# Performance work log

Hardware: AMD Instinct MI355X
Metric: run time of the kernel (lower is better)

## Reference

```python
import jax, jax.numpy as jnp
import numpy as np

D = 2048        # hidden_size
F = 1024        # moe_intermediate_size
E = 16          # num_experts
TOP_K = 2       # num_experts_per_tok
NORM_TOPK = True
B, S = 2, 1024


def setup_inputs() -> dict:
    key = jax.random.key(0)
    ks = jax.random.split(key, 6)
    scale = 0.02
    x = jax.random.normal(ks[0], (B, S, D), jnp.float32)
    w_gate = jax.random.normal(ks[1], (D, E), jnp.float32) * scale          # gate Linear (no bias)
    w_g = jax.random.normal(ks[2], (E, D, F), jnp.float32) * scale          # SwitchGLU gate_proj
    w_u = jax.random.normal(ks[3], (E, D, F), jnp.float32) * scale          # SwitchGLU up_proj
    w_d = jax.random.normal(ks[4], (E, F, D), jnp.float32) * scale          # SwitchGLU down_proj
    expert_bias = jnp.zeros((E,), jnp.float32)                              # nn.Parameter(zeros)
    return {"x": x, "w_gate": w_gate, "w_g": w_g, "w_u": w_u, "w_d": w_d,
            "expert_bias": expert_bias}


def reference(x, w_gate, w_g, w_u, w_d, expert_bias):
    xf = x.reshape(-1, D)  # [T, D] flatten tokens
    T = xf.shape[0]
    # routing: softmax in fp32, bias added AFTER softmax (as in source)
    gates = jax.nn.softmax((xf @ w_gate).astype(jnp.float32), axis=-1) + expert_bias
    scores, inds = jax.lax.top_k(gates, TOP_K)  # values gathered from biased gates
    if NORM_TOPK:
        scores = scores / (jnp.sum(scores, axis=-1, keepdims=True) + 1e-20)
    scores = scores.astype(x.dtype)
    # scatter top-k weights into dense [T, E] combine matrix (top-k inds are distinct)
    cw = jnp.zeros((T, E), x.dtype).at[jnp.arange(T)[:, None], inds].add(scores)
    # scan over experts: each step one gated-SiLU MLP + weighted accumulate
    def step(acc, inp):
        wg, wu, wd, w = inp  # wg/wu [D,F], wd [F,D], w [T]
        h = jax.nn.silu(xf @ wg) * (xf @ wu)  # [T, F]
        return acc + w[:, None] * (h @ wd), None
    y, _ = jax.lax.scan(step, jnp.zeros_like(xf), (w_g, w_u, w_d, cw.T))
    return y.reshape(x.shape)
```

## Files before the change

kernel.cpp:

```cpp
#include <hip/hip_runtime.h>
#include <hip/hip_bf16.h>

#define D_DIM 2048
#define F_DIM 1024
#define E_NUM 16
#define T_TOK 2048
#define NSLOT (T_TOK * 2)

typedef float f32x4 __attribute__((ext_vector_type(4)));
typedef short short8 __attribute__((ext_vector_type(8)));

__device__ inline unsigned pk2bf(float a, float b) {
    __hip_bfloat162 h2 = __float22bfloat162_rn(make_float2(a, b));
    union { __hip_bfloat162 h; unsigned u; } c; c.h = h2; return c.u;
}

__global__ __launch_bounds__(64) void k_route(const float* __restrict__ x,
                                              const float* __restrict__ wg,
                                              const float* __restrict__ bias,
                                              int* __restrict__ topk_idx,
                                              float* __restrict__ topk_w,
                                              int* __restrict__ counts) {
    int t = blockIdx.x;
    int l = threadIdx.x;
    int e = l & 15, c = l >> 4;
    const float* xr = x + (size_t)t * D_DIM + c * (D_DIM / 4);
    const float* wr = wg + (size_t)(c * (D_DIM / 4)) * E_NUM + e;
    float acc = 0.f;
#pragma unroll 4
    for (int d = 0; d < D_DIM / 4; ++d) acc += xr[d] * wr[(size_t)d * E_NUM];
    acc += __shfl_xor(acc, 16);
    acc += __shfl_xor(acc, 32);
    float m = acc;
#pragma unroll
    for (int s = 1; s < 16; s <<= 1) m = fmaxf(m, __shfl_xor(m, s));
    float p = __expf(acc - m);
    float sum = p;
#pragma unroll
    for (int s = 1; s < 16; s <<= 1) sum += __shfl_xor(sum, s);
    p = p / sum + bias[e];
    float v1 = p; int i1 = e;
#pragma unroll
    for (int s = 1; s < 16; s <<= 1) {
        float ov = __shfl_xor(v1, s); int oi = __shfl_xor(i1, s);
        if (ov > v1 || (ov == v1 && oi < i1)) { v1 = ov; i1 = oi; }
    }
    float v2 = (e == i1) ? -1e30f : p; int i2 = e;
#pragma unroll
    for (int s = 1; s < 16; s <<= 1) {
        float ov = __shfl_xor(v2, s); int oi = __shfl_xor(i2, s);
        if (ov > v2 || (ov == v2 && oi < i2)) { v2 = ov; i2 = oi; }
    }
    if (l == 0) {
        float s2 = v1 + v2 + 1e-20f;
        topk_idx[2 * t] = i1; topk_idx[2 * t + 1] = i2;
        topk_w[2 * t] = v1 / s2; topk_w[2 * t + 1] = v2 / s2;
        atomicAdd(&counts[i1], 1);
        atomicAdd(&counts[i2], 1);
    }
}

__global__ void k_offsets(const int* __restrict__ counts, int* __restrict__ offsets,
                          int* __restrict__ cursors) {
    if (threadIdx.x == 0) {
        int run = 0;
        for (int e = 0; e < E_NUM; ++e) { offsets[e] = run; cursors[e] = run; run += counts[e]; }
        offsets[E_NUM] = run;
    }
}

__global__ void k_scatter(const int* __restrict__ topk_idx, const float* __restrict__ topk_w,
                          int* __restrict__ cursors, int* __restrict__ token_ids,
                          float* __restrict__ slot_w) {
    int i = blockIdx.x * blockDim.x + threadIdx.x;
    if (i >= NSLOT) return;
    int e = topk_idx[i];
    int slot = atomicAdd(&cursors[e], 1);
    token_ids[slot] = i >> 1;
    slot_w[slot] = topk_w[i];
}

__global__ __launch_bounds__(256) void k_gather(const float* __restrict__ x,
                                                const int* __restrict__ token_ids,
                                                __hip_bfloat16* __restrict__ xg) {
    int s = blockIdx.x;
    const float* src = x + (size_t)token_ids[s] * D_DIM + threadIdx.x * 8;
    f32x4 a = *(const f32x4*)src;
    f32x4 b = *(const f32x4*)(src + 4);
    union { short8 v; unsigned u[4]; } w;
    w.u[0] = pk2bf(a.x, a.y); w.u[1] = pk2bf(a.z, a.w);
    w.u[2] = pk2bf(b.x, b.y); w.u[3] = pk2bf(b.z, b.w);
    *(short8*)((unsigned short*)xg + (size_t)s * D_DIM + threadIdx.x * 8) = w.v;
}

__global__ __launch_bounds__(256, 4) void k_gateup(const __hip_bfloat16* __restrict__ xg,
                                                   const float* __restrict__ wg_all,
                                                   const float* __restrict__ wu_all,
                                                   const int* __restrict__ offsets,
                                                   __hip_bfloat16* __restrict__ hbuf) {
    unsigned b0 = blockIdx.x;
    unsigned w = (b0 & 7) * 1024u + (b0 >> 3);
    int mi = w & 31;
    int ni = (w >> 5) & 15;
    int e  = w >> 9;
    int off = offsets[e];
    int n_e = offsets[e + 1] - off;
    int m0 = mi * 64;
    if (m0 >= n_e) return;
    int n0 = ni * 64;
    const float* wg = wg_all + (size_t)e * (D_DIM * F_DIM);
    const float* wu = wu_all + (size_t)e * (D_DIM * F_DIM);

    __shared__ unsigned short As[2][64 * 40];
    __shared__ unsigned short Bs[2][2][64 * 40];

    int tid = threadIdx.x;
    int wid = tid >> 6, lane = tid & 63;
    int q = lane >> 4, nl = lane & 15;
    int wr = wid >> 1, wc = wid & 1;

    int arow = tid >> 2, acg = (tid & 3) * 8;
    int sg = off + m0 + arow; if (sg > NSLOT - 1) sg = NSLOT - 1;
    const unsigned short* xrow = (const unsigned short*)xg + (size_t)sg * D_DIM;
    int bkr = (tid >> 4) * 2;
    int bcol = (tid & 15) * 4;

    short8 rA;
    f32x4 rg[2], ru[2];
    f32x4 accG[2][2], accU[2][2];
#pragma unroll
    for (int ms = 0; ms < 2; ++ms)
#pragma unroll
        for (int ns = 0; ns < 2; ++ns) {
            accG[ms][ns] = (f32x4){0.f, 0.f, 0.f, 0.f};
            accU[ms][ns] = (f32x4){0.f, 0.f, 0.f, 0.f};
        }

    auto loadG = [&](int k0) {
        rA = *(const short8*)(xrow + k0 + acg);
        size_t o0 = (size_t)(k0 + bkr) * F_DIM + n0 + bcol;
        rg[0] = *(const f32x4*)(wg + o0);
        rg[1] = *(const f32x4*)(wg + o0 + F_DIM);
        ru[0] = *(const f32x4*)(wu + o0);
        ru[1] = *(const f32x4*)(wu + o0 + F_DIM);
    };
    auto writeL = [&](int b) {
        *(short8*)&As[b][arow * 40 + acg] = rA;
#pragma unroll
        for (int j = 0; j < 4; ++j) {
            int col = bcol + j;
            int kk = bkr ^ (((col >> 3) & 3) << 3);
            *(unsigned*)&Bs[b][0][col * 40 + kk] = pk2bf(rg[0][j], rg[1][j]);
            *(unsigned*)&Bs[b][1][col * 40 + kk] = pk2bf(ru[0][j], ru[1][j]);
        }
    };
    auto compute = [&](int b) {
        short8 af[2];
#pragma unroll
        for (int ms = 0; ms < 2; ++ms)
            af[ms] = *(const short8*)&As[b][(wr * 32 + ms * 16 + nl) * 40 + q * 8];
#pragma unroll
        for (int ns = 0; ns < 2; ++ns) {
            int col = wc * 32 + ns * 16 + nl;
            int colb = col * 40 + 8 * (q ^ ((col >> 3) & 3));
            short8 bg = *(const short8*)&Bs[b][0][colb];
            short8 bu = *(const short8*)&Bs[b][1][colb];
#pragma unroll
            for (int ms = 0; ms < 2; ++ms) {
                accG[ms][ns] = __builtin_amdgcn_mfma_f32_16x16x32_bf16(af[ms], bg, accG[ms][ns], 0, 0, 0);
                accU[ms][ns] = __builtin_amdgcn_mfma_f32_16x16x32_bf16(af[ms], bu, accU[ms][ns], 0, 0, 0);
            }
        }
    };

    loadG(0);
    writeL(0);
    __syncthreads();
    for (int t = 0; t < D_DIM / 32; ++t) {
        int b = t & 1;
        if (t < D_DIM / 32 - 1) loadG((t + 1) * 32);
        compute(b);
        if (t < D_DIM / 32 - 1) writeL(b ^ 1);
        __syncthreads();
    }

#pragma unroll
    for (int ms = 0; ms < 2; ++ms)
#pragma unroll
        for (int j = 0; j < 4; ++j) {
            int g2 = m0 + wr * 32 + ms * 16 + q * 4 + j;
            if (g2 < n_e) {
                size_t hbase = (size_t)(off + g2) * F_DIM;
#pragma unroll
                for (int ns = 0; ns < 2; ++ns) {
                    float g = accG[ms][ns][j];
                    float u = accU[ms][ns][j];
                    float hv = (g / (1.f + __expf(-g))) * u;
                    hbuf[hbase + n0 + wc * 32 + ns * 16 + nl] = __float2bfloat16(hv);
                }
            }
        }
}

__global__ __launch_bounds__(256, 4) void k_down(const __hip_bfloat16* __restrict__ hbuf,
                                                 const float* __restrict__ wd_all,
                                                 const int* __restrict__ offsets,
                                                 const int* __restrict__ token_ids,
                                                 const float* __restrict__ slot_w,
                                                 float* __restrict__ y) {
    unsigned b0 = blockIdx.x;
    unsigned w = (b0 & 7) * 2048u + (b0 >> 3);
    int mi = w & 31;
    int ni = (w >> 5) & 31;
    int e  = w >> 10;
    int off = offsets[e];
    int n_e = offsets[e + 1] - off;
    int m0 = mi * 64;
    if (m0 >= n_e) return;
    int n0 = ni * 64;
    const float* wd = wd_all + (size_t)e * (F_DIM * D_DIM);

    __shared__ unsigned short As[2][64 * 40];
    __shared__ unsigned short Bs[2][64 * 40];

    int tid = threadIdx.x;
    int wid = tid >> 6, lane = tid & 63;
    int q = lane >> 4, nl = lane & 15;
    int wr = wid >> 1, wc = wid & 1;

    int arow = tid >> 2, acg = (tid & 3) * 8;
    int sg = off + m0 + arow; if (sg > NSLOT - 1) sg = NSLOT - 1;
    const unsigned short* hrow = (const unsigned short*)hbuf + (size_t)sg * F_DIM;
    int bkr = (tid >> 4) * 2;
    int bcol = (tid & 15) * 4;

    short8 rh;
    f32x4 rd[2];
    f32x4 acc[2][2];
#pragma unroll
    for (int ms = 0; ms < 2; ++ms)
#pragma unroll
        for (int ns = 0; ns < 2; ++ns) acc[ms][ns] = (f32x4){0.f, 0.f, 0.f, 0.f};

    auto loadG = [&](int k0) {
        rh = *(const short8*)(hrow + k0 + acg);
        size_t o0 = (size_t)(k0 + bkr) * D_DIM + n0 + bcol;
        rd[0] = *(const f32x4*)(wd + o0);
        rd[1] = *(const f32x4*)(wd + o0 + D_DIM);
    };
    auto writeL = [&](int b) {
        *(short8*)&As[b][arow * 40 + acg] = rh;
#pragma unroll
        for (int j = 0; j < 4; ++j) {
            int col = bcol + j;
            int kk = bkr ^ (((col >> 3) & 3) << 3);
            *(unsigned*)&Bs[b][col * 40 + kk] = pk2bf(rd[0][j], rd[1][j]);
        }
    };
    auto compute = [&](int b) {
        short8 af[2];
#pragma unroll
        for (int ms = 0; ms < 2; ++ms)
            af[ms] = *(const short8*)&As[b][(wr * 32 + ms * 16 + nl) * 40 + q * 8];
#pragma unroll
        for (int ns = 0; ns < 2; ++ns) {
            int col = wc * 32 + ns * 16 + nl;
            short8 bd = *(const short8*)&Bs[b][col * 40 + 8 * (q ^ ((col >> 3) & 3))];
#pragma unroll
            for (int ms = 0; ms < 2; ++ms)
                acc[ms][ns] = __builtin_amdgcn_mfma_f32_16x16x32_bf16(af[ms], bd, acc[ms][ns], 0, 0, 0);
        }
    };

    loadG(0);
    writeL(0);
    __syncthreads();
    for (int t = 0; t < F_DIM / 32; ++t) {
        int b = t & 1;
        if (t < F_DIM / 32 - 1) loadG((t + 1) * 32);
        compute(b);
        if (t < F_DIM / 32 - 1) writeL(b ^ 1);
        __syncthreads();
    }

#pragma unroll
    for (int ms = 0; ms < 2; ++ms)
#pragma unroll
        for (int j = 0; j < 4; ++j) {
            int g2 = m0 + wr * 32 + ms * 16 + q * 4 + j;
            if (g2 < n_e) {
                float w2 = slot_w[off + g2];
                int t = token_ids[off + g2];
#pragma unroll
                for (int ns = 0; ns < 2; ++ns)
                    atomicAdd(&y[(size_t)t * D_DIM + n0 + wc * 32 + ns * 16 + nl], acc[ms][ns][j] * w2);
            }
        }
}

extern "C" void kernel_launch(void* const* d_in, const int* in_sizes, int n_in,
                              void* d_out, int out_size, void* d_ws, size_t ws_size,
                              hipStream_t stream) {
    const float* x      = (const float*)d_in[0];
    const float* w_gate = (const float*)d_in[1];
    const float* w_g    = (const float*)d_in[2];
    const float* w_u    = (const float*)d_in[3];
    const float* w_d    = (const float*)d_in[4];
    const float* bias   = (const float*)d_in[5];
    float* y = (float*)d_out;

    char* ws = (char*)d_ws;
    int*   counts    = (int*)(ws + 0);
    int*   offsets   = (int*)(ws + 64);
    int*   cursors   = (int*)(ws + 192);
    int*   topk_idx  = (int*)(ws + 256);
    float* topk_w    = (float*)(ws + 256 + 16384);
    int*   token_ids = (int*)(ws + 256 + 32768);
    float* slot_w    = (float*)(ws + 256 + 49152);
    __hip_bfloat16* hbuf = (__hip_bfloat16*)(ws + 66048);
    __hip_bfloat16* xg   = (__hip_bfloat16*)(ws + 66048 + 8388608);

    hipMemsetAsync(ws, 0, 256, stream);
    hipMemsetAsync(d_out, 0, (size_t)out_size * sizeof(float), stream);

    k_route<<<T_TOK, 64, 0, stream>>>(x, w_gate, bias, topk_idx, topk_w, counts);
    k_offsets<<<1, 64, 0, stream>>>(counts, offsets, cursors);
    k_scatter<<<(NSLOT + 255) / 256, 256, 0, stream>>>(topk_idx, topk_w, cursors, token_ids, slot_w);
    k_gather<<<NSLOT, 256, 0, stream>>>(x, token_ids, xg);
    k_gateup<<<16 * 32 * E_NUM, 256, 0, stream>>>(xg, w_g, w_u, offsets, hbuf);
    k_down<<<32 * 32 * E_NUM, 256, 0, stream>>>(hbuf, w_d, offsets, token_ids, slot_w, y);
}
```

Measured before the change: 375.2 us.

## Pre-convert weights and activations to tiled bf16 images with direct-to-LDS loads

Adds prep kernels that transpose and convert the fp32 expert weights into bf16 tile images laid out per (expert, n-tile, k-step). They also pack the gathered tokens into per-128-row tile images. New gate/up and down GEMM kernels stream these contiguous tiles straight into LDS with global_load_lds, using 128-row M tiles and a compact list of non-empty blocks. This drops the in-loop fp32->bf16 conversion and the strided weight loads. The cost is an extra weight-conversion pass each call (about 400MB read plus 200MB written) and a large workspace, with the old path kept as a fallback when the workspace is too small.

```diff
diff --git a/kernel.cpp b/kernel.cpp
--- a/kernel.cpp
+++ b/kernel.cpp
@@ -9,10 +9,23 @@
 
 typedef float f32x4 __attribute__((ext_vector_type(4)));
 typedef short short8 __attribute__((ext_vector_type(8)));
+typedef unsigned uint2v __attribute__((ext_vector_type(2)));
 
 __device__ inline unsigned pk2bf(float a, float b) {
     __hip_bfloat162 h2 = __float22bfloat162_rn(make_float2(a, b));
     union { __hip_bfloat162 h; unsigned u; } c; c.h = h2; return c.u;
+}
+
+__device__ inline unsigned short bf16bits(float a) {
+    union { __hip_bfloat16 h; unsigned short u; } c;
+    c.h = __float2bfloat16(a);
+    return c.u;
+}
+
+typedef __attribute__((address_space(1))) const unsigned int* gas_p;
+typedef __attribute__((address_space(3))) unsigned int* las_p;
+__device__ __forceinline__ void gld16(const unsigned short* g, unsigned short* l) {
+    __builtin_amdgcn_global_load_lds((gas_p)(const void*)g, (las_p)(void*)l, 16, 0, 0);
 }
 
 __global__ __launch_bounds__(64) void k_route(const float* __restrict__ x,
@@ -61,11 +74,19 @@
 }
 
 __global__ void k_offsets(const int* __restrict__ counts, int* __restrict__ offsets,
-                          int* __restrict__ cursors) {
+                          int* __restrict__ cursors, int* __restrict__ pbe,
+                          int* __restrict__ pbm, int* __restrict__ npbp) {
     if (threadIdx.x == 0) {
-        int run = 0;
-        for (int e = 0; e < E_NUM; ++e) { offsets[e] = run; cursors[e] = run; run += counts[e]; }
+        int run = 0, npb = 0;
+        for (int e = 0; e < E_NUM; ++e) {
+            offsets[e] = run; cursors[e] = run;
+            int ne = counts[e];
+            int nb = (ne + 127) >> 7;
+            for (int i = 0; i < nb; ++i) { pbe[npb] = e; pbm[npb] = i; ++npb; }
+            run += ne;
+        }
         offsets[E_NUM] = run;
+        npbp[0] = npb;
     }
 }
 
@@ -80,9 +101,238 @@
     slot_w[slot] = topk_w[i];
 }
 
-__global__ __launch_bounds__(256) void k_gather(const float* __restrict__ x,
-                                                const int* __restrict__ token_ids,
-                                                __hip_bfloat16* __restrict__ xg) {
+__global__ __launch_bounds__(256) void k_gatherI(const float* __restrict__ x,
+                                                 const int* __restrict__ token_ids,
+                                                 const int* __restrict__ offsets,
+                                                 const int* __restrict__ pbe,
+                                                 const int* __restrict__ pbm,
+                                                 const int* __restrict__ npbp,
+                                                 unsigned short* __restrict__ xgI) {
+    int pb = blockIdx.y;
+    if (pb >= npbp[0]) return;
+    int ks = blockIdx.x;
+    int e = pbe[pb];
+    int ne = offsets[e + 1] - offsets[e];
+    int t = threadIdx.x;
+    int r = t >> 1, half = (t & 1) * 16;
+    int local = pbm[pb] * 128 + r;
+    unsigned o[8];
+    if (local < ne) {
+        const float* src = x + (size_t)token_ids[offsets[e] + local] * D_DIM + ks * 32 + half;
+        f32x4 a = *(const f32x4*)src;
+        f32x4 b = *(const f32x4*)(src + 4);
+        f32x4 c = *(const f32x4*)(src + 8);
+        f32x4 d = *(const f32x4*)(src + 12);
+        o[0] = pk2bf(a.x, a.y); o[1] = pk2bf(a.z, a.w);
+        o[2] = pk2bf(b.x, b.y); o[3] = pk2bf(b.z, b.w);
+        o[4] = pk2bf(c.x, c.y); o[5] = pk2bf(c.z, c.w);
+        o[6] = pk2bf(d.x, d.y); o[7] = pk2bf(d.z, d.w);
+    } else {
+#pragma unroll
+        for (int i = 0; i < 8; ++i) o[i] = 0;
+    }
+    unsigned short* dst = xgI + ((size_t)(pb * 64 + ks)) * 4096 + r * 32 + half;
+    union { short8 v; unsigned u[4]; } w0, w1;
+    w0.u[0] = o[0]; w0.u[1] = o[1]; w0.u[2] = o[2]; w0.u[3] = o[3];
+    w1.u[0] = o[4]; w1.u[1] = o[5]; w1.u[2] = o[6]; w1.u[3] = o[7];
+    *(short8*)dst = w0.v;
+    *(short8*)(dst + 8) = w1.v;
+}
+
+__global__ __launch_bounds__(256) void k_prep_gu(const float* __restrict__ wg_all,
+                                                 const float* __restrict__ wu_all,
+                                                 unsigned short* __restrict__ wguI) {
+    int ks = blockIdx.x, n = blockIdx.y, e = blockIdx.z;
+    __shared__ float S[32][40];
+    int t = threadIdx.x;
+    int kk = t >> 3, cg = (t & 7) * 4;
+    int col = t >> 3, k4 = (t & 7) * 4;
+    size_t rbase = (size_t)e * (D_DIM * F_DIM) + (size_t)(ks * 32) * F_DIM + n * 32;
+    unsigned short* obase = wguI + ((size_t)((e * 32 + n) * 64 + ks)) * 2048;
+    const float* mats[2] = { wg_all, wu_all };
+#pragma unroll
+    for (int m = 0; m < 2; ++m) {
+        *(f32x4*)&S[kk][cg] = *(const f32x4*)(mats[m] + rbase + (size_t)kk * F_DIM + cg);
+        __syncthreads();
+        uint2v o;
+        o[0] = pk2bf(S[k4][col], S[k4 + 1][col]);
+        o[1] = pk2bf(S[k4 + 2][col], S[k4 + 3][col]);
+        *(uint2v*)&obase[m * 1024 + col * 32 + k4] = o;
+        __syncthreads();
+    }
+}
+
+__global__ __launch_bounds__(256) void k_prep_d(const float* __restrict__ wd_all,
+                                                unsigned short* __restrict__ wdI) {
+    int ks = blockIdx.x, n = blockIdx.y, e = blockIdx.z;
+    __shared__ float S[32][68];
+    int t = threadIdx.x;
+    int kk = t >> 3, cg = (t & 7) * 8;
+    int col = t >> 2, k8 = (t & 3) * 8;
+    size_t rbase = (size_t)e * (F_DIM * D_DIM) + (size_t)(ks * 32) * D_DIM + n * 64;
+    unsigned short* obase = wdI + ((size_t)((e * 32 + n) * 32 + ks)) * 2048;
+    const float* src = wd_all + rbase + (size_t)kk * D_DIM + cg;
+    *(f32x4*)&S[kk][cg] = *(const f32x4*)src;
+    *(f32x4*)&S[kk][cg + 4] = *(const f32x4*)(src + 4);
+    __syncthreads();
+    union { short8 v; unsigned u[4]; } o;
+#pragma unroll
+    for (int i = 0; i < 4; ++i)
+        o.u[i] = pk2bf(S[k8 + 2 * i][col], S[k8 + 2 * i + 1][col]);
+    *(short8*)&obase[col * 32 + k8] = o.v;
+}
+
+__global__ __launch_bounds__(256, 6) void k_gateupI(const unsigned short* __restrict__ xgI,
+                                                    const unsigned short* __restrict__ wguI,
+                                                    const int* __restrict__ pbe,
+                                                    const int* __restrict__ npbp,
+                                                    unsigned short* __restrict__ hI) {
+    int pb = blockIdx.y;
+    if (pb >= npbp[0]) return;
+    int n = blockIdx.x;
+    int e = pbe[pb];
+    __shared__ __align__(16) unsigned short A[2][4096];
+    __shared__ __align__(16) unsigned short B[2][2048];
+    int tid = threadIdx.x, wid = tid >> 6, lane = tid & 63;
+    int q = lane >> 4, nl = lane & 15;
+    const unsigned short* abase = xgI + (size_t)pb * (64 * 4096);
+    const unsigned short* bbase = wguI + ((size_t)((e * 32 + n) * 64)) * 2048;
+
+    f32x4 accG[2][2], accU[2][2];
+#pragma unroll
+    for (int ms = 0; ms < 2; ++ms)
+#pragma unroll
+        for (int ns = 0; ns < 2; ++ns) {
+            accG[ms][ns] = (f32x4){0.f, 0.f, 0.f, 0.f};
+            accU[ms][ns] = (f32x4){0.f, 0.f, 0.f, 0.f};
+        }
+
+    auto STAGE = [&](int buf, int ks) {
+        const unsigned short* at = abase + (size_t)ks * 4096;
+        const unsigned short* bt = bbase + (size_t)ks * 2048;
+        gld16(at + (wid * 2) * 512 + lane * 8, &A[buf][(wid * 2) * 512]);
+        gld16(at + (wid * 2 + 1) * 512 + lane * 8, &A[buf][(wid * 2 + 1) * 512]);
+        gld16(bt + wid * 512 + lane * 8, &B[buf][wid * 512]);
+    };
+    auto COMP = [&](int buf) {
+        short8 af[2];
+#pragma unroll
+        for (int ms = 0; ms < 2; ++ms)
+            af[ms] = *(const short8*)&A[buf][(wid * 32 + ms * 16 + nl) * 32 + q * 8];
+#pragma unroll
+        for (int ns = 0; ns < 2; ++ns) {
+            int col = ns * 16 + nl;
+            short8 bg = *(const short8*)&B[buf][col * 32 + q * 8];
+            short8 bu = *(const short8*)&B[buf][1024 + col * 32 + q * 8];
+#pragma unroll
+            for (int ms = 0; ms < 2; ++ms) {
+                accG[ms][ns] = __builtin_amdgcn_mfma_f32_16x16x32_bf16(af[ms], bg, accG[ms][ns], 0, 0, 0);
+                accU[ms][ns] = __builtin_amdgcn_mfma_f32_16x16x32_bf16(af[ms], bu, accU[ms][ns], 0, 0, 0);
+            }
+        }
+    };
+
+    STAGE(0, 0);
+    __syncthreads();
+    for (int t = 0; t < 64; ++t) {
+        if (t < 63) STAGE((t & 1) ^ 1, t + 1);
+        COMP(t & 1);
+        __syncthreads();
+    }
+
+#pragma unroll
+    for (int ms = 0; ms < 2; ++ms)
+#pragma unroll
+        for (int j = 0; j < 4; ++j) {
+            int r = wid * 32 + ms * 16 + q * 4 + j;
+#pragma unroll
+            for (int ns = 0; ns < 2; ++ns) {
+                float g = accG[ms][ns][j];
+                float u = accU[ms][ns][j];
+                float hv = (g / (1.f + __expf(-g))) * u;
+                hI[((size_t)(pb * 32 + n)) * 4096 + r * 32 + ns * 16 + nl] = bf16bits(hv);
+            }
+        }
+}
+
+__global__ __launch_bounds__(256, 6) void k_downI(const unsigned short* __restrict__ hI,
+                                                  const unsigned short* __restrict__ wdI,
+                                                  const int* __restrict__ offsets,
+                                                  const int* __restrict__ pbe,
+                                                  const int* __restrict__ pbm,
+                                                  const int* __restrict__ npbp,
+                                                  const int* __restrict__ token_ids,
+                                                  const float* __restrict__ slot_w,
+                                                  float* __restrict__ y) {
+    int pb = blockIdx.y;
+    if (pb >= npbp[0]) return;
+    int n = blockIdx.x;
+    int e = pbe[pb];
+    int off = offsets[e];
+    int ne = offsets[e + 1] - off;
+    __shared__ __align__(16) unsigned short A[2][4096];
+    __shared__ __align__(16) unsigned short B[2][2048];
+    int tid = threadIdx.x, wid = tid >> 6, lane = tid & 63;
+    int q = lane >> 4, nl = lane & 15;
+    int wr = wid >> 1, wc = wid & 1;
+    const unsigned short* abase = hI + (size_t)pb * (32 * 4096);
+    const unsigned short* bbase = wdI + ((size_t)((e * 32 + n) * 32)) * 2048;
+
+    f32x4 acc[4][2];
+#pragma unroll
+    for (int ms = 0; ms < 4; ++ms)
+#pragma unroll
+        for (int ns = 0; ns < 2; ++ns) acc[ms][ns] = (f32x4){0.f, 0.f, 0.f, 0.f};
+
+    auto STAGE = [&](int buf, int ks) {
+        const unsigned short* at = abase + (size_t)ks * 4096;
+        const unsigned short* bt = bbase + (size_t)ks * 2048;
+        gld16(at + (wid * 2) * 512 + lane * 8, &A[buf][(wid * 2) * 512]);
+        gld16(at + (wid * 2 + 1) * 512 + lane * 8, &A[buf][(wid * 2 + 1) * 512]);
+        gld16(bt + wid * 512 + lane * 8, &B[buf][wid * 512]);
+    };
+    auto COMP = [&](int buf) {
+        short8 af[4];
+#pragma unroll
+        for (int ms = 0; ms < 4; ++ms)
+            af[ms] = *(const short8*)&A[buf][(wr * 64 + ms * 16 + nl) * 32 + q * 8];
+#pragma unroll
+        for (int ns = 0; ns < 2; ++ns) {
+            int col = wc * 32 + ns * 16 + nl;
+            short8 bd = *(const short8*)&B[buf][col * 32 + q * 8];
+#pragma unroll
+            for (int ms = 0; ms < 4; ++ms)
+                acc[ms][ns] = __builtin_amdgcn_mfma_f32_16x16x32_bf16(af[ms], bd, acc[ms][ns], 0, 0, 0);
+        }
+    };
+
+    STAGE(0, 0);
+    __syncthreads();
+    for (int t = 0; t < 32; ++t) {
+        if (t < 31) STAGE((t & 1) ^ 1, t + 1);
+        COMP(t & 1);
+        __syncthreads();
+    }
+
+#pragma unroll
+    for (int ms = 0; ms < 4; ++ms)
+#pragma unroll
+        for (int j = 0; j < 4; ++j) {
+            int r = wr * 64 + ms * 16 + q * 4 + j;
+            int local = pbm[pb] * 128 + r;
+            if (local < ne) {
+                float w2 = slot_w[off + local];
+                int tok = token_ids[off + local];
+#pragma unroll
+                for (int ns = 0; ns < 2; ++ns)
+                    atomicAdd(&y[(size_t)tok * D_DIM + n * 64 + wc * 32 + ns * 16 + nl], acc[ms][ns][j] * w2);
+            }
+        }
+}
+
+__global__ __launch_bounds__(256) void k_gather_fb(const float* __restrict__ x,
+                                                   const int* __restrict__ token_ids,
+                                                   __hip_bfloat16* __restrict__ xg) {
     int s = blockIdx.x;
     const float* src = x + (size_t)token_ids[s] * D_DIM + threadIdx.x * 8;
     f32x4 a = *(const f32x4*)src;
@@ -93,11 +343,11 @@
     *(short8*)((unsigned short*)xg + (size_t)s * D_DIM + threadIdx.x * 8) = w.v;
 }
 
-__global__ __launch_bounds__(256, 4) void k_gateup(const __hip_bfloat16* __restrict__ xg,
-                                                   const float* __restrict__ wg_all,
-                                                   const float* __restrict__ wu_all,
-                                                   const int* __restrict__ offsets,
-                                                   __hip_bfloat16* __restrict__ hbuf) {
+__global__ __launch_bounds__(256, 4) void k_gateup_fb(const __hip_bfloat16* __restrict__ xg,
+                                                      const float* __restrict__ wg_all,
+                                                      const float* __restrict__ wu_all,
+                                                      const int* __restrict__ offsets,
+                                                      __hip_bfloat16* __restrict__ hbuf) {
     unsigned b0 = blockIdx.x;
     unsigned w = (b0 & 7) * 1024u + (b0 >> 3);
     int mi = w & 31;
@@ -110,21 +360,17 @@
     int n0 = ni * 64;
     const float* wg = wg_all + (size_t)e * (D_DIM * F_DIM);
     const float* wu = wu_all + (size_t)e * (D_DIM * F_DIM);
-
     __shared__ unsigned short As[2][64 * 40];
     __shared__ unsigned short Bs[2][2][64 * 40];
-
     int tid = threadIdx.x;
     int wid = tid >> 6, lane = tid & 63;
     int q = lane >> 4, nl = lane & 15;
     int wr = wid >> 1, wc = wid & 1;
-
     int arow = tid >> 2, acg = (tid & 3) * 8;
     int sg = off + m0 + arow; if (sg > NSLOT - 1) sg = NSLOT - 1;
     const unsigned short* xrow = (const unsigned short*)xg + (size_t)sg * D_DIM;
     int bkr = (tid >> 4) * 2;
     int bcol = (tid & 15) * 4;
-
     short8 rA;
     f32x4 rg[2], ru[2];
     f32x4 accG[2][2], accU[2][2];
@@ -135,7 +381,6 @@
             accG[ms][ns] = (f32x4){0.f, 0.f, 0.f, 0.f};
             accU[ms][ns] = (f32x4){0.f, 0.f, 0.f, 0.f};
         }
-
     auto loadG = [&](int k0) {
         rA = *(const short8*)(xrow + k0 + acg);
         size_t o0 = (size_t)(k0 + bkr) * F_DIM + n0 + bcol;
@@ -172,9 +417,7 @@
             }
         }
     };
-
-    loadG(0);
-    writeL(0);
+    loadG(0); writeL(0);
     __syncthreads();
     for (int t = 0; t < D_DIM / 32; ++t) {
         int b = t & 1;
@@ -183,7 +426,6 @@
         if (t < D_DIM / 32 - 1) writeL(b ^ 1);
         __syncthreads();
     }
-
 #pragma unroll
     for (int ms = 0; ms < 2; ++ms)
 #pragma unroll
@@ -202,12 +444,12 @@
         }
 }
 
-__global__ __launch_bounds__(256, 4) void k_down(const __hip_bfloat16* __restrict__ hbuf,
-                                                 const float* __restrict__ wd_all,
-                                                 const int* __restrict__ offsets,
-                                                 const int* __restrict__ token_ids,
-                                                 const float* __restrict__ slot_w,
-                                                 float* __restrict__ y) {
+__global__ __launch_bounds__(256, 4) void k_down_fb(const __hip_bfloat16* __restrict__ hbuf,
+                                                    const float* __restrict__ wd_all,
+                                                    const int* __restrict__ offsets,
+                                                    const int* __restrict__ token_ids,
+                                                    const float* __restrict__ slot_w,
+                                                    float* __restrict__ y) {
     unsigned b0 = blockIdx.x;
     unsigned w = (b0 & 7) * 2048u + (b0 >> 3);
     int mi = w & 31;
@@ -219,21 +461,17 @@
     if (m0 >= n_e) return;
     int n0 = ni * 64;
     const float* wd = wd_all + (size_t)e * (F_DIM * D_DIM);
-
     __shared__ unsigned short As[2][64 * 40];
     __shared__ unsigned short Bs[2][64 * 40];
-
     int tid = threadIdx.x;
     int wid = tid >> 6, lane = tid & 63;
     int q = lane >> 4, nl = lane & 15;
     int wr = wid >> 1, wc = wid & 1;
-
     int arow = tid >> 2, acg = (tid & 3) * 8;
     int sg = off + m0 + arow; if (sg > NSLOT - 1) sg = NSLOT - 1;
     const unsigned short* hrow = (const unsigned short*)hbuf + (size_t)sg * F_DIM;
     int bkr = (tid >> 4) * 2;
     int bcol = (tid & 15) * 4;
-
     short8 rh;
     f32x4 rd[2];
     f32x4 acc[2][2];
@@ -241,7 +479,6 @@
     for (int ms = 0; ms < 2; ++ms)
 #pragma unroll
         for (int ns = 0; ns < 2; ++ns) acc[ms][ns] = (f32x4){0.f, 0.f, 0.f, 0.f};
-
     auto loadG = [&](int k0) {
         rh = *(const short8*)(hrow + k0 + acg);
         size_t o0 = (size_t)(k0 + bkr) * D_DIM + n0 + bcol;
@@ -271,9 +508,7 @@
                 acc[ms][ns] = __builtin_amdgcn_mfma_f32_16x16x32_bf16(af[ms], bd, acc[ms][ns], 0, 0, 0);
         }
     };
-
-    loadG(0);
-    writeL(0);
+    loadG(0); writeL(0);
     __syncthreads();
     for (int t = 0; t < F_DIM / 32; ++t) {
         int b = t & 1;
@@ -282,7 +517,6 @@
         if (t < F_DIM / 32 - 1) writeL(b ^ 1);
         __syncthreads();
     }
-
 #pragma unroll
     for (int ms = 0; ms < 2; ++ms)
 #pragma unroll
@@ -313,20 +547,39 @@
     int*   counts    = (int*)(ws + 0);
     int*   offsets   = (int*)(ws + 64);
     int*   cursors   = (int*)(ws + 192);
-    int*   topk_idx  = (int*)(ws + 256);
-    float* topk_w    = (float*)(ws + 256 + 16384);
-    int*   token_ids = (int*)(ws + 256 + 32768);
-    float* slot_w    = (float*)(ws + 256 + 49152);
-    __hip_bfloat16* hbuf = (__hip_bfloat16*)(ws + 66048);
-    __hip_bfloat16* xg   = (__hip_bfloat16*)(ws + 66048 + 8388608);
-
-    hipMemsetAsync(ws, 0, 256, stream);
+    int*   pbe       = (int*)(ws + 256);
+    int*   pbm       = (int*)(ws + 512);
+    int*   npbp      = (int*)(ws + 768);
+    int*   topk_idx  = (int*)(ws + 1024);
+    float* topk_w    = (float*)(ws + 17408);
+    int*   token_ids = (int*)(ws + 33792);
+    float* slot_w    = (float*)(ws + 50176);
+
+    const size_t IMG0 = 66560;
+    unsigned short* xgI  = (unsigned short*)(ws + IMG0);
+    unsigned short* hI   = (unsigned short*)(ws + IMG0 + 25165824);
+    unsigned short* wguI = (unsigned short*)(ws + IMG0 + 37748736);
+    unsigned short* wdI  = (unsigned short*)(ws + IMG0 + 171966464);
+    const size_t NEED = IMG0 + 171966464 + 67108864;
+
+    hipMemsetAsync(ws, 0, 1024, stream);
     hipMemsetAsync(d_out, 0, (size_t)out_size * sizeof(float), stream);
 
     k_route<<<T_TOK, 64, 0, stream>>>(x, w_gate, bias, topk_idx, topk_w, counts);
-    k_offsets<<<1, 64, 0, stream>>>(counts, offsets, cursors);
+    k_offsets<<<1, 64, 0, stream>>>(counts, offsets, cursors, pbe, pbm, npbp);
     k_scatter<<<(NSLOT + 255) / 256, 256, 0, stream>>>(topk_idx, topk_w, cursors, token_ids, slot_w);
-    k_gather<<<NSLOT, 256, 0, stream>>>(x, token_ids, xg);
-    k_gateup<<<16 * 32 * E_NUM, 256, 0, stream>>>(xg, w_g, w_u, offsets, hbuf);
-    k_down<<<32 * 32 * E_NUM, 256, 0, stream>>>(hbuf, w_d, offsets, token_ids, slot_w, y);
-}
+
+    if (ws_size >= NEED) {
+        k_gatherI<<<dim3(64, 48), 256, 0, stream>>>(x, token_ids, offsets, pbe, pbm, npbp, xgI);
+        k_prep_gu<<<dim3(64, 32, 16), 256, 0, stream>>>(w_g, w_u, wguI);
+        k_prep_d<<<dim3(32, 32, 16), 256, 0, stream>>>(w_d, wdI);
+        k_gateupI<<<dim3(32, 48), 256, 0, stream>>>(xgI, wguI, pbe, npbp, hI);
+        k_downI<<<dim3(32, 48), 256, 0, stream>>>(hI, wdI, offsets, pbe, pbm, npbp, token_ids, slot_w, y);
+    } else {
+        __hip_bfloat16* hbuf = (__hip_bfloat16*)(ws + IMG0);
+        __hip_bfloat16* xg   = (__hip_bfloat16*)(ws + IMG0 + 8388608);
+        k_gather_fb<<<NSLOT, 256, 0, stream>>>(x, token_ids, xg);
+        k_gateup_fb<<<16 * 32 * E_NUM, 256, 0, stream>>>(xg, w_g, w_u, offsets, hbuf);
+        k_down_fb<<<32 * 32 * E_NUM, 256, 0, stream>>>(hbuf, w_d, offsets, token_ids, slot_w, y);
+    }
+}
```

Result: no change. 371.3 us (-1.0%).
